# Kernel optimization log

Hardware: AMD Instinct MI355X
Metric: run time of the kernel (lower is better)

The kernel has to match this reference:

```python
import jax, jax.numpy as jnp
import numpy as np
from jax.scipy.special import ndtr

TABLE_RANGE = 128
LRELU_SLOPE = 0.2


def ste_round(x):
    # round(x) - detach(x) + x : straight-through estimator (eval path uses floor(x+0.5))
    return x + jax.lax.stop_gradient(jnp.floor(x + 0.5) - x)


def block_sample(x, masked):
    """Faithful, efficient version of BlockSample's sparse one-hot 7x7 conv.
    out[b, k*16+i*4+j, y, x] = in[b, k, y+i-3, x+j-2]  (zeros outside; masked kills (i=3,j>=2)).
    Equivalent to gathering 4x4 patches from the input padded by 3, at offset (i, j+1).
    Returns (b*h*w, c, 4, 4)."""
    b, c, h, w = x.shape
    xp = jnp.pad(x, ((0, 0), (0, 0), (3, 3), (3, 3)))
    # 16 static shifted slices -> (b, c, 4, 4, h, w)
    patches = jnp.stack(
        [xp[:, :, i:i + h, j + 1:j + 1 + w] for i in range(4) for j in range(4)], axis=2
    ).reshape(b, c, 4, 4, h, w)
    if masked:
        m = np.ones((4, 4), dtype=np.float32)
        m[3, 2] = 0.0
        m[3, 3] = 0.0
        patches = patches * jnp.asarray(m)[None, None, :, :, None, None]
    # (b, h, w, c, 4, 4) -> (b*h*w, c, 4, 4)
    return patches.transpose(0, 4, 5, 1, 2, 3).reshape(b * h * w, c, 4, 4)


def conv2d(x, w, b, stride):
    y = jax.lax.conv_general_dilated(
        x, w, (stride, stride), ((1, 1), (1, 1)),
        dimension_numbers=('NCHW', 'OIHW', 'NCHW'))
    return y + b[None, :, None, None]


def lrelu(x):
    return jnp.where(x >= 0, x, LRELU_SLOPE * x)


def setup_inputs() -> dict:
    key = jax.random.key(0)
    ks = jax.random.split(key, 8)
    b, c, ch, h, w, dim = 8, 192, 192, 32, 48, 192
    y = jax.random.normal(ks[0], (b, c, h, w), jnp.float32) * 4.0
    h_tilde = jax.random.normal(ks[1], (b, ch, h, w), jnp.float32)
    s = 0.02
    w0 = jax.random.normal(ks[2], (dim, c + ch, 3, 3), jnp.float32) * s
    b0 = jnp.zeros((dim,), jnp.float32)
    w1 = jax.random.normal(ks[3], (dim, dim, 3, 3), jnp.float32) * s
    b1 = jnp.zeros((dim,), jnp.float32)
    w2 = jax.random.normal(ks[4], (dim, dim, 3, 3), jnp.float32) * s
    b2 = jnp.zeros((dim,), jnp.float32)
    fc_w = jax.random.normal(ks[5], (2 * c, dim * 2 * 2), jnp.float32) * s
    fc_b = jnp.zeros((2 * c,), jnp.float32)
    return {'y': y, 'h_tilde': h_tilde, 'w0': w0, 'b0': b0, 'w1': w1, 'b1': b1,
            'w2': w2, 'b2': b2, 'fc_w': fc_w, 'fc_b': fc_b}


def reference(y, h_tilde, w0, b0, w1, b1, w2, b2, fc_w, fc_b):
    b, c, h, w = y.shape
    # quantize latents (NoiseQuant eval path with STE gradient)
    y_q = jnp.clip(ste_round(y), -TABLE_RANGE, TABLE_RANGE - 1)
    ys = block_sample(y_q, masked=True)        # (b*h*w, c, 4, 4)
    hs = block_sample(h_tilde, masked=False)   # (b*h*w, ch, 4, 4)
    merged = jnp.concatenate([ys, hs], axis=1)
    # PredictionModel_Context.transform
    t = lrelu(conv2d(merged, w0, b0, 1))       # (N, dim, 4, 4)
    t = lrelu(conv2d(t, w1, b1, 2))            # (N, dim, 2, 2)
    t = lrelu(conv2d(t, w2, b2, 1))            # (N, dim, 2, 2)
    ctx = t.reshape(t.shape[0], -1) @ fc_w.T + fc_b  # (N, 2c)
    hyper_mu = ctx[:, :c].reshape(b, h, w, c).transpose(0, 3, 1, 2)
    hyper_sigma = jnp.exp(ctx[:, c:]).reshape(b, h, w, c).transpose(0, 3, 1, 2)
    # GaussianModel: CDF(upper) - CDF(lower), clamped
    upper = (y_q - hyper_mu + 0.5) / hyper_sigma
    lower = (y_q - hyper_mu - 0.5) / hyper_sigma
    likelihood = jnp.clip(ndtr(upper) - ndtr(lower), 1e-12, None)
    return likelihood
```

## Files before the change

### kernel.cpp

```cpp
#include <hip/hip_runtime.h>
#include <math.h>

constexpr int Bb   = 8;
constexpr int Cc   = 192;
constexpr int Hh   = 32;
constexpr int Ww   = 48;
constexpr int NPIX = 1536;
constexpr int S    = 12288;

typedef __attribute__((ext_vector_type(8))) short s16x8;
typedef __attribute__((ext_vector_type(4))) float f32x4;
typedef unsigned short u16;

#define LRELU(v) ((v) >= 0.0f ? (v) : 0.2f * (v))

__device__ __forceinline__ u16 f2b(float x) {
    __bf16 h = (__bf16)x;
    return *reinterpret_cast<u16*>(&h);
}

__global__ __launch_bounds__(256) void k_quantT(
    const float* __restrict__ y, const float* __restrict__ ht,
    u16* __restrict__ XT)
{
    __shared__ float ld[32][33];
    const int tx = threadIdx.x, ty = threadIdx.y;
    const int p0 = blockIdx.x * 32, c0 = blockIdx.y * 32;
    const int img = blockIdx.z >> 1, src = blockIdx.z & 1;
    const float* sp = (src ? ht : y) + (size_t)img * 192 * NPIX;
    #pragma unroll
    for (int k = 0; k < 4; ++k) {
        float v = sp[(size_t)(c0 + ty + 8 * k) * NPIX + p0 + tx];
        if (!src) v = fminf(fmaxf(floorf(v + 0.5f), -128.0f), 127.0f);
        ld[ty + 8 * k][tx] = v;
    }
    __syncthreads();
    #pragma unroll
    for (int k = 0; k < 4; ++k)
        XT[((size_t)img * NPIX + p0 + ty + 8 * k) * 384 + src * 192 + c0 + tx] =
            f2b(ld[tx][ty + 8 * k]);
}

__global__ void k_prep_w0nk(const float* __restrict__ w, u16* __restrict__ wt) {
    int i = blockIdx.x * 256 + threadIdx.x;
    if (i >= 1728 * 384) return;
    int n = i / 384, ic = i % 384;
    int k = n / 192, oc = n % 192;
    wt[i] = f2b(w[(oc * 384 + ic) * 9 + k]);
}
__global__ void k_prep_w1pk(const float* __restrict__ w, u16* __restrict__ wt) {
    const int posflat[25] = {0,1,4,5, 1,2,3,5,6,7, 4,5,8,9,12,13,
                             5,6,7,9,10,11,13,14,15};
    int i = blockIdx.x * 256 + threadIdx.x;
    if (i >= 921600) return;
    int z, r, K, sbase;
    if      (i < 147456) { z = 0; r = i;          K = 768;  sbase = 0;  }
    else if (i < 368640) { z = 1; r = i - 147456; K = 1152; sbase = 4;  }
    else if (i < 589824) { z = 2; r = i - 368640; K = 1152; sbase = 10; }
    else                 { z = 3; r = i - 589824; K = 1728; sbase = 16; }
    int n = r / K, k = r % K;
    int slab = k / 192, ic = k % 192;
    int pos = posflat[sbase + slab];
    int py = pos >> 2, px = pos & 3;
    int ki = py - 2 * (z >> 1) + 1, kj = px - 2 * (z & 1) + 1;
    wt[i] = f2b(w[(n * 192 + ic) * 9 + ki * 3 + kj]);
}
__global__ void k_prep_w2pk(const float* __restrict__ w, u16* __restrict__ wt) {
    int i = blockIdx.x * 256 + threadIdx.x;
    if (i >= 589824) return;
    int z = i / 147456, r = i % 147456;
    int n = r / 768, k = r % 768;
    int pos = k / 192, ic = k % 192;
    int ki = (pos >> 1) - (z >> 1) + 1, kj = (pos & 1) - (z & 1) + 1;
    wt[i] = f2b(w[(n * 192 + ic) * 9 + ki * 3 + kj]);
}
__global__ void k_prep_fcpk(const float* __restrict__ w, u16* __restrict__ wt) {
    int i = blockIdx.x * 256 + threadIdx.x;
    if (i >= 384 * 768) return;
    int o = i / 768, fp = i % 768;
    int q = fp / 192, oc = fp % 192;
    wt[i] = f2b(w[o * 768 + oc * 4 + q]);
}

__global__ __launch_bounds__(256) void k_hgemm(
    const u16* __restrict__ XT, const u16* __restrict__ W,
    float* __restrict__ Hf, float* __restrict__ Hy)
{
    __shared__ u16 As[128 * 40];
    __shared__ u16 Bs[64 * 40];
    const int tid = threadIdx.x;
    const int wave = tid >> 6, lane = tid & 63;
    const int wm = wave >> 1, wn = wave & 1;
    const int l15 = lane & 15, lk = lane >> 4;
    const int n0 = blockIdx.x * 64, s0 = blockIdx.y * 128;

    f32x4 acc[4][2], snap[4][2];
    #pragma unroll
    for (int a = 0; a < 4; ++a)
        #pragma unroll
        for (int b = 0; b < 2; ++b) { acc[a][b] = (f32x4){0,0,0,0}; snap[a][b] = (f32x4){0,0,0,0}; }

    for (int k0 = 0; k0 < 384; k0 += 32) {
        if (k0 == 192) {
            #pragma unroll
            for (int a = 0; a < 4; ++a)
                #pragma unroll
                for (int b = 0; b < 2; ++b) snap[a][b] = acc[a][b];
        }
        #pragma unroll
        for (int i = tid; i < 768; i += 256) {
            if (i < 512) {
                int row = i >> 2, c = i & 3;
                *reinterpret_cast<uint4*>(&As[row * 40 + c * 8]) =
                    *reinterpret_cast<const uint4*>(&XT[(size_t)(s0 + row) * 384 + k0 + c * 8]);
            } else {
                int j = i - 512, row = j >> 2, c = j & 3;
                *reinterpret_cast<uint4*>(&Bs[row * 40 + c * 8]) =
                    *reinterpret_cast<const uint4*>(&W[(size_t)(n0 + row) * 384 + k0 + c * 8]);
            }
        }
        __syncthreads();
        s16x8 af[4], bf[2];
        #pragma unroll
        for (int mi = 0; mi < 4; ++mi)
            af[mi] = *reinterpret_cast<const s16x8*>(&As[(wm * 64 + mi * 16 + l15) * 40 + lk * 8]);
        #pragma unroll
        for (int ni = 0; ni < 2; ++ni)
            bf[ni] = *reinterpret_cast<const s16x8*>(&Bs[(wn * 32 + ni * 16 + l15) * 40 + lk * 8]);
        #pragma unroll
        for (int mi = 0; mi < 4; ++mi)
            #pragma unroll
            for (int ni = 0; ni < 2; ++ni)
                acc[mi][ni] = __builtin_amdgcn_mfma_f32_16x16x32_bf16(af[mi], bf[ni], acc[mi][ni], 0, 0, 0);
        __syncthreads();
    }
    #pragma unroll
    for (int mi = 0; mi < 4; ++mi)
        #pragma unroll
        for (int r = 0; r < 4; ++r) {
            int srow = s0 + wm * 64 + mi * 16 + lk * 4 + r;
            #pragma unroll
            for (int ni = 0; ni < 2; ++ni) {
                int nc = n0 + wn * 32 + ni * 16 + l15;
                Hf[(size_t)srow * 1728 + nc] = acc[mi][ni][r];
                if (n0 >= 576) Hy[(size_t)srow * 1152 + nc - 576] = snap[mi][ni][r];
            }
        }
}

struct TDm { int K[4]; int woff[4]; int yoff[4]; int pm[4][9]; };

__global__ __launch_bounds__(256) void k_mgemm(
    const u16* __restrict__ X, int sx,
    const u16* __restrict__ Wb, const float* __restrict__ bias,
    void* __restrict__ Yb, int sy, int mode, TDm d)
{
    __shared__ u16 As[128 * 40];
    __shared__ u16 Bs[64 * 40];
    const int z = blockIdx.z;
    const int K = d.K[z];
    const u16* W = Wb + d.woff[z];
    const int tid = threadIdx.x;
    const int wave = tid >> 6, lane = tid & 63;
    const int wm = wave >> 1, wn = wave & 1;
    const int l15 = lane & 15, lk = lane >> 4;
    const int n0 = blockIdx.x * 64, s0 = blockIdx.y * 128;

    f32x4 acc[4][2];
    #pragma unroll
    for (int a = 0; a < 4; ++a)
        #pragma unroll
        for (int b = 0; b < 2; ++b) acc[a][b] = (f32x4){0,0,0,0};

    for (int k0 = 0; k0 < K; k0 += 32) {
        const int colA0 = d.pm[z][k0 / 192] * 192 + (k0 % 192);
        #pragma unroll
        for (int i = tid; i < 768; i += 256) {
            if (i < 512) {
                int row = i >> 2, c = i & 3;
                *reinterpret_cast<uint4*>(&As[row * 40 + c * 8]) =
                    *reinterpret_cast<const uint4*>(&X[(size_t)(s0 + row) * sx + colA0 + c * 8]);
            } else {
                int j = i - 512, row = j >> 2, c = j & 3;
                *reinterpret_cast<uint4*>(&Bs[row * 40 + c * 8]) =
                    *reinterpret_cast<const uint4*>(&W[(size_t)(n0 + row) * K + k0 + c * 8]);
            }
        }
        __syncthreads();
        s16x8 af[4], bf[2];
        #pragma unroll
        for (int mi = 0; mi < 4; ++mi)
            af[mi] = *reinterpret_cast<const s16x8*>(&As[(wm * 64 + mi * 16 + l15) * 40 + lk * 8]);
        #pragma unroll
        for (int ni = 0; ni < 2; ++ni)
            bf[ni] = *reinterpret_cast<const s16x8*>(&Bs[(wn * 32 + ni * 16 + l15) * 40 + lk * 8]);
        #pragma unroll
        for (int mi = 0; mi < 4; ++mi)
            #pragma unroll
            for (int ni = 0; ni < 2; ++ni)
                acc[mi][ni] = __builtin_amdgcn_mfma_f32_16x16x32_bf16(af[mi], bf[ni], acc[mi][ni], 0, 0, 0);
        __syncthreads();
    }
    #pragma unroll
    for (int mi = 0; mi < 4; ++mi)
        #pragma unroll
        for (int r = 0; r < 4; ++r) {
            int srow = s0 + wm * 64 + mi * 16 + lk * 4 + r;
            #pragma unroll
            for (int ni = 0; ni < 2; ++ni) {
                int nc = n0 + wn * 32 + ni * 16 + l15;
                float v = acc[mi][ni][r] + bias[nc];
                if (mode == 0) {
                    v = LRELU(v);
                    ((u16*)Yb)[(size_t)srow * sy + d.yoff[z] + nc] = f2b(v);
                } else {
                    ((float*)Yb)[(size_t)srow * sy + d.yoff[z] + nc] = v;
                }
            }
        }
}

__global__ __launch_bounds__(192) void k_asm(
    const float* __restrict__ Hf, const float* __restrict__ Hy,
    const float* __restrict__ b0, u16* __restrict__ t0)
{
    const int cpx = gridDim.x >> 3;
    const int bid = (blockIdx.x & 7) * cpx + (blockIdx.x >> 3);
    const int oc = threadIdx.x;
    const float bias = b0[oc];
    for (int si = 0; si < 8; ++si) {
        const int s = bid * 8 + si;
        const int imgbase = (s / NPIX) * NPIX;
        const int p = s % NPIX;
        const int yy = p / Ww, xx = p % Ww;
        float acc[16];
        #pragma unroll
        for (int i = 0; i < 16; ++i) acc[i] = bias;
        #pragma unroll
        for (int py = 0; py < 4; ++py) {
            #pragma unroll
            for (int px = 0; px < 4; ++px) {
                int Y = yy + py - 3, X = xx + px - 2;
                if ((unsigned)Y < (unsigned)Hh && (unsigned)X < (unsigned)Ww) {
                    const float* hp = Hf + (size_t)(imgbase + Y * Ww + X) * 1728 + oc;
                    #pragma unroll
                    for (int dy = -1; dy <= 1; ++dy) {
                        int oy = py - dy; if (oy < 0 || oy > 3) continue;
                        #pragma unroll
                        for (int dx = -1; dx <= 1; ++dx) {
                            int ox = px - dx; if (ox < 0 || ox > 3) continue;
                            acc[oy * 4 + ox] += hp[((dy + 1) * 3 + dx + 1) * 192];
                        }
                    }
                }
            }
        }
        {
            const float* yp = Hy + (size_t)s * 1152 + oc;
            #pragma unroll
            for (int dy = 0; dy <= 1; ++dy)
                #pragma unroll
                for (int dx = -1; dx <= 1; ++dx)
                    acc[(3 - dy) * 4 + (2 - dx)] -= yp[(dy * 3 + dx + 1) * 192];
        }
        if (xx + 1 < Ww) {
            const float* yp = Hy + (size_t)(s + 1) * 1152 + oc;
            #pragma unroll
            for (int dy = 0; dy <= 1; ++dy)
                #pragma unroll
                for (int dx = 0; dx <= 1; ++dx)
                    acc[(3 - dy) * 4 + (3 - dx)] -= yp[(dy * 3 + dx + 1) * 192];
        }
        u16* tr = t0 + (size_t)s * 3072 + oc;
        #pragma unroll
        for (int pos = 0; pos < 16; ++pos) tr[pos * 192] = f2b(LRELU(acc[pos]));
    }
}

__global__ void k_like(const float* __restrict__ ctx, const u16* __restrict__ XT,
                       float* __restrict__ like)
{
    int i = blockIdx.x * 256 + threadIdx.x;
    if (i >= 192 * S) return;
    int s = i / 192, c = i % 192;
    u16 qb = XT[(size_t)s * 384 + c];
    unsigned qu = (unsigned)qb << 16;
    float q  = __uint_as_float(qu);
    float mu = ctx[(size_t)s * 384 + c];
    float sg = expf(ctx[(size_t)s * 384 + 192 + c]);
    float inv = 1.0f / sg;
    float up = (q - mu + 0.5f) * inv;
    float lo = (q - mu - 0.5f) * inv;
    const float kc = 0.70710678118654752f;
    float lk = 0.5f * erfcf(-up * kc) - 0.5f * erfcf(-lo * kc);
    like[i] = fmaxf(lk, 1e-12f);
}

__global__ __launch_bounds__(256) void k_outT(
    const float* __restrict__ like, float* __restrict__ out)
{
    __shared__ float ld[32][33];
    const int tx = threadIdx.x, ty = threadIdx.y;
    const int p0 = blockIdx.x * 32, c0 = blockIdx.y * 32;
    const int img = blockIdx.z;
    #pragma unroll
    for (int k = 0; k < 4; ++k)
        ld[ty + 8 * k][tx] = like[((size_t)img * NPIX + p0 + ty + 8 * k) * 192 + c0 + tx];
    __syncthreads();
    #pragma unroll
    for (int k = 0; k < 4; ++k)
        out[((size_t)img * 192 + c0 + ty + 8 * k) * NPIX + p0 + tx] = ld[tx][ty + 8 * k];
}

extern "C" void kernel_launch(void* const* d_in, const int* in_sizes, int n_in,
                              void* d_out, int out_size, void* d_ws, size_t ws_size,
                              hipStream_t stream) {
    const float* y    = (const float*)d_in[0];
    const float* ht   = (const float*)d_in[1];
    const float* w0   = (const float*)d_in[2];
    const float* b0   = (const float*)d_in[3];
    const float* w1   = (const float*)d_in[4];
    const float* b1   = (const float*)d_in[5];
    const float* w2   = (const float*)d_in[6];
    const float* b2   = (const float*)d_in[7];
    const float* fcw  = (const float*)d_in[8];
    const float* fcb  = (const float*)d_in[9];
    float* out = (float*)d_out;

    char* ws = (char*)d_ws;
    u16*   XT   = (u16*)(ws);
    u16*   w0nk = (u16*)(ws + 9437184);
    u16*   w1pk = (u16*)(ws + 10764288);
    u16*   w2pk = (u16*)(ws + 12607488);
    u16*   fcpk = (u16*)(ws + 13787136);
    float* Hf   = (float*)(ws + 14376960);
    float* Hy   = (float*)(ws + 99311616);
    u16*   t0   = (u16*)(ws + 155934720);
    u16*   t1   = (u16*)Hy;
    u16*   t2   = (u16*)(ws + 99311616 + 18874368);
    float* ctx  = Hf;
    float* like = (float*)(ws + 14376960 + 18874368);

    k_quantT<<<dim3(48, 6, 16), dim3(32, 8), 0, stream>>>(y, ht, XT);
    k_prep_w0nk<<<(1728 * 384 + 255) / 256, 256, 0, stream>>>(w0, w0nk);
    k_prep_w1pk<<<(921600 + 255) / 256, 256, 0, stream>>>(w1, w1pk);
    k_prep_w2pk<<<(589824 + 255) / 256, 256, 0, stream>>>(w2, w2pk);
    k_prep_fcpk<<<(384 * 768 + 255) / 256, 256, 0, stream>>>(fcw, fcpk);

    TDm dB = {}, dC = {}, dD = {};
    const int KB[4]   = {768, 1152, 1152, 1728};
    const int wB[4]   = {0, 147456, 368640, 589824};
    const int pmB[4][9] = {
        {0,1,4,5,0,0,0,0,0},
        {1,2,3,5,6,7,0,0,0},
        {4,5,8,9,12,13,0,0,0},
        {5,6,7,9,10,11,13,14,15}};
    for (int q = 0; q < 4; ++q) {
        dB.K[q] = KB[q]; dB.woff[q] = wB[q]; dB.yoff[q] = q * 192;
        for (int j = 0; j < 9; ++j) dB.pm[q][j] = pmB[q][j];
        dC.K[q] = 768; dC.woff[q] = q * 147456; dC.yoff[q] = q * 192;
        for (int j = 0; j < 4; ++j) dC.pm[q][j] = j;
        dD.K[q] = 768; dD.woff[q] = 0; dD.yoff[q] = 0;
        for (int j = 0; j < 4; ++j) dD.pm[q][j] = j;
    }

    k_hgemm<<<dim3(27, 96), 256, 0, stream>>>(XT, w0nk, Hf, Hy);
    k_asm<<<1536, 192, 0, stream>>>(Hf, Hy, b0, t0);
    k_mgemm<<<dim3(3, 96, 4), 256, 0, stream>>>(t0, 3072, w1pk, b1, t1, 768, 0, dB);
    k_mgemm<<<dim3(3, 96, 4), 256, 0, stream>>>(t1, 768, w2pk, b2, t2, 768, 0, dC);
    k_mgemm<<<dim3(6, 96, 1), 256, 0, stream>>>(t2, 768, fcpk, fcb, ctx, 384, 1, dD);
    k_like<<<(192 * S + 255) / 256, 256, 0, stream>>>(ctx, XT, like);
    k_outT<<<dim3(48, 6, 8), dim3(32, 8), 0, stream>>>(like, out);
}
```

Baseline: 413.9 us.

## Widen GEMM tiles with direct-to-LDS loads and store conv0 partials in bf16

The shared GEMM kernel now uses 128x192 tiles with K steps of 64 and an XOR-swizzled LDS layout. Tiles are filled with global_load_lds direct-to-LDS copies instead of register staging. The separate conv0 GEMM is replaced by two launches of the generic GEMM, one for the full-K partials and one for the y-only partials with its own weight pack. Both write bf16 instead of fp32, and the assembly kernel reads packed bf16 pairs, which halves that intermediate traffic. The second conv is merged into one wide-N launch with a replicated bias. This cuts memory traffic and raises reuse per tile, at the cost of more register pressure, larger LDS use and bf16 rounding of the partial sums.

```diff
diff --git a/kernel.cpp b/kernel.cpp
--- a/kernel.cpp
+++ b/kernel.cpp
@@ -11,12 +11,19 @@
 typedef __attribute__((ext_vector_type(8))) short s16x8;
 typedef __attribute__((ext_vector_type(4))) float f32x4;
 typedef unsigned short u16;
+typedef unsigned int   u32;
 
 #define LRELU(v) ((v) >= 0.0f ? (v) : 0.2f * (v))
 
 __device__ __forceinline__ u16 f2b(float x) {
     __bf16 h = (__bf16)x;
     return *reinterpret_cast<u16*>(&h);
+}
+
+__device__ __forceinline__ void gload(const u16* g, u16* l) {
+    __builtin_amdgcn_global_load_lds(
+        (const __attribute__((address_space(1))) unsigned int*)g,
+        (__attribute__((address_space(3))) unsigned int*)l, 16, 0, 0);
 }
 
 __global__ __launch_bounds__(256) void k_quantT(
@@ -46,6 +53,13 @@
     if (i >= 1728 * 384) return;
     int n = i / 384, ic = i % 384;
     int k = n / 192, oc = n % 192;
+    wt[i] = f2b(w[(oc * 384 + ic) * 9 + k]);
+}
+__global__ void k_prep_w0yk(const float* __restrict__ w, u16* __restrict__ wt) {
+    int i = blockIdx.x * 256 + threadIdx.x;
+    if (i >= 1152 * 192) return;
+    int n = i / 192, ic = i % 192;
+    int oc = n % 192, k = n / 192 + 3;
     wt[i] = f2b(w[(oc * 384 + ic) * 9 + k]);
 }
 __global__ void k_prep_w1pk(const float* __restrict__ w, u16* __restrict__ wt) {
@@ -81,71 +95,9 @@
     int q = fp / 192, oc = fp % 192;
     wt[i] = f2b(w[o * 768 + oc * 4 + q]);
 }
-
-__global__ __launch_bounds__(256) void k_hgemm(
-    const u16* __restrict__ XT, const u16* __restrict__ W,
-    float* __restrict__ Hf, float* __restrict__ Hy)
-{
-    __shared__ u16 As[128 * 40];
-    __shared__ u16 Bs[64 * 40];
-    const int tid = threadIdx.x;
-    const int wave = tid >> 6, lane = tid & 63;
-    const int wm = wave >> 1, wn = wave & 1;
-    const int l15 = lane & 15, lk = lane >> 4;
-    const int n0 = blockIdx.x * 64, s0 = blockIdx.y * 128;
-
-    f32x4 acc[4][2], snap[4][2];
-    #pragma unroll
-    for (int a = 0; a < 4; ++a)
-        #pragma unroll
-        for (int b = 0; b < 2; ++b) { acc[a][b] = (f32x4){0,0,0,0}; snap[a][b] = (f32x4){0,0,0,0}; }
-
-    for (int k0 = 0; k0 < 384; k0 += 32) {
-        if (k0 == 192) {
-            #pragma unroll
-            for (int a = 0; a < 4; ++a)
-                #pragma unroll
-                for (int b = 0; b < 2; ++b) snap[a][b] = acc[a][b];
-        }
-        #pragma unroll
-        for (int i = tid; i < 768; i += 256) {
-            if (i < 512) {
-                int row = i >> 2, c = i & 3;
-                *reinterpret_cast<uint4*>(&As[row * 40 + c * 8]) =
-                    *reinterpret_cast<const uint4*>(&XT[(size_t)(s0 + row) * 384 + k0 + c * 8]);
-            } else {
-                int j = i - 512, row = j >> 2, c = j & 3;
-                *reinterpret_cast<uint4*>(&Bs[row * 40 + c * 8]) =
-                    *reinterpret_cast<const uint4*>(&W[(size_t)(n0 + row) * 384 + k0 + c * 8]);
-            }
-        }
-        __syncthreads();
-        s16x8 af[4], bf[2];
-        #pragma unroll
-        for (int mi = 0; mi < 4; ++mi)
-            af[mi] = *reinterpret_cast<const s16x8*>(&As[(wm * 64 + mi * 16 + l15) * 40 + lk * 8]);
-        #pragma unroll
-        for (int ni = 0; ni < 2; ++ni)
-            bf[ni] = *reinterpret_cast<const s16x8*>(&Bs[(wn * 32 + ni * 16 + l15) * 40 + lk * 8]);
-        #pragma unroll
-        for (int mi = 0; mi < 4; ++mi)
-            #pragma unroll
-            for (int ni = 0; ni < 2; ++ni)
-                acc[mi][ni] = __builtin_amdgcn_mfma_f32_16x16x32_bf16(af[mi], bf[ni], acc[mi][ni], 0, 0, 0);
-        __syncthreads();
-    }
-    #pragma unroll
-    for (int mi = 0; mi < 4; ++mi)
-        #pragma unroll
-        for (int r = 0; r < 4; ++r) {
-            int srow = s0 + wm * 64 + mi * 16 + lk * 4 + r;
-            #pragma unroll
-            for (int ni = 0; ni < 2; ++ni) {
-                int nc = n0 + wn * 32 + ni * 16 + l15;
-                Hf[(size_t)srow * 1728 + nc] = acc[mi][ni][r];
-                if (n0 >= 576) Hy[(size_t)srow * 1152 + nc - 576] = snap[mi][ni][r];
-            }
-        }
+__global__ void k_prep_b2rep(const float* __restrict__ b, float* __restrict__ o) {
+    int i = blockIdx.x * 256 + threadIdx.x;
+    if (i < 768) o[i] = b[i % 192];
 }
 
 struct TDm { int K[4]; int woff[4]; int yoff[4]; int pm[4][9]; };
@@ -155,125 +107,155 @@
     const u16* __restrict__ Wb, const float* __restrict__ bias,
     void* __restrict__ Yb, int sy, int mode, TDm d)
 {
-    __shared__ u16 As[128 * 40];
-    __shared__ u16 Bs[64 * 40];
+    __shared__ u16 As[128 * 64];
+    __shared__ u16 Bs[192 * 64];
     const int z = blockIdx.z;
     const int K = d.K[z];
     const u16* W = Wb + d.woff[z];
     const int tid = threadIdx.x;
-    const int wave = tid >> 6, lane = tid & 63;
-    const int wm = wave >> 1, wn = wave & 1;
+    const int wv = tid >> 6, lane = tid & 63;
+    const int wm = wv & 1, wn = wv >> 1;
     const int l15 = lane & 15, lk = lane >> 4;
-    const int n0 = blockIdx.x * 64, s0 = blockIdx.y * 128;
-
-    f32x4 acc[4][2];
+    const int lr = lane >> 3, lc = lane & 7;
+    const int sc = lc ^ lr;
+    const int n0 = blockIdx.x * 192, s0 = blockIdx.y * 128;
+
+    f32x4 acc[4][6];
     #pragma unroll
     for (int a = 0; a < 4; ++a)
         #pragma unroll
-        for (int b = 0; b < 2; ++b) acc[a][b] = (f32x4){0,0,0,0};
-
-    for (int k0 = 0; k0 < K; k0 += 32) {
-        const int colA0 = d.pm[z][k0 / 192] * 192 + (k0 % 192);
-        #pragma unroll
-        for (int i = tid; i < 768; i += 256) {
-            if (i < 512) {
-                int row = i >> 2, c = i & 3;
-                *reinterpret_cast<uint4*>(&As[row * 40 + c * 8]) =
-                    *reinterpret_cast<const uint4*>(&X[(size_t)(s0 + row) * sx + colA0 + c * 8]);
+        for (int b = 0; b < 6; ++b) acc[a][b] = (f32x4){0, 0, 0, 0};
+
+    int slab = 0, kin = 0;
+    for (int k0 = 0; k0 < K; k0 += 64) {
+        const int colA0 = d.pm[z][slab] * 192 + kin;
+        for (int st = wv; st < 40; st += 4) {
+            if (st < 16) {
+                const u16* g = X + (size_t)(s0 + st * 8 + lr) * sx + colA0 + sc * 8;
+                gload(g, &As[st * 512]);
             } else {
-                int j = i - 512, row = j >> 2, c = j & 3;
-                *reinterpret_cast<uint4*>(&Bs[row * 40 + c * 8]) =
-                    *reinterpret_cast<const uint4*>(&W[(size_t)(n0 + row) * K + k0 + c * 8]);
+                const int bs = st - 16;
+                const u16* g = W + (size_t)(n0 + bs * 8 + lr) * K + k0 + sc * 8;
+                gload(g, &Bs[bs * 512]);
             }
         }
         __syncthreads();
-        s16x8 af[4], bf[2];
-        #pragma unroll
-        for (int mi = 0; mi < 4; ++mi)
-            af[mi] = *reinterpret_cast<const s16x8*>(&As[(wm * 64 + mi * 16 + l15) * 40 + lk * 8]);
-        #pragma unroll
-        for (int ni = 0; ni < 2; ++ni)
-            bf[ni] = *reinterpret_cast<const s16x8*>(&Bs[(wn * 32 + ni * 16 + l15) * 40 + lk * 8]);
-        #pragma unroll
-        for (int mi = 0; mi < 4; ++mi)
-            #pragma unroll
-            for (int ni = 0; ni < 2; ++ni)
-                acc[mi][ni] = __builtin_amdgcn_mfma_f32_16x16x32_bf16(af[mi], bf[ni], acc[mi][ni], 0, 0, 0);
+
+        #pragma unroll
+        for (int ks = 0; ks < 2; ++ks) {
+            s16x8 af[4], bf[6];
+            #pragma unroll
+            for (int mi = 0; mi < 4; ++mi) {
+                const int r = wm * 64 + mi * 16 + l15;
+                af[mi] = *reinterpret_cast<const s16x8*>(
+                    &As[r * 64 + (((ks * 4 + lk) * 8) ^ ((l15 & 7) << 3))]);
+            }
+            #pragma unroll
+            for (int ni = 0; ni < 6; ++ni) {
+                const int r = wn * 96 + ni * 16 + l15;
+                bf[ni] = *reinterpret_cast<const s16x8*>(
+                    &Bs[r * 64 + (((ks * 4 + lk) * 8) ^ ((l15 & 7) << 3))]);
+            }
+            #pragma unroll
+            for (int mi = 0; mi < 4; ++mi)
+                #pragma unroll
+                for (int ni = 0; ni < 6; ++ni)
+                    acc[mi][ni] = __builtin_amdgcn_mfma_f32_16x16x32_bf16(
+                        af[mi], bf[ni], acc[mi][ni], 0, 0, 0);
+        }
         __syncthreads();
+        kin += 64; if (kin == 192) { kin = 0; ++slab; }
     }
+
     #pragma unroll
     for (int mi = 0; mi < 4; ++mi)
         #pragma unroll
         for (int r = 0; r < 4; ++r) {
-            int srow = s0 + wm * 64 + mi * 16 + lk * 4 + r;
-            #pragma unroll
-            for (int ni = 0; ni < 2; ++ni) {
-                int nc = n0 + wn * 32 + ni * 16 + l15;
-                float v = acc[mi][ni][r] + bias[nc];
+            const int srow = s0 + wm * 64 + mi * 16 + lk * 4 + r;
+            #pragma unroll
+            for (int ni = 0; ni < 6; ++ni) {
+                const int ng = n0 + wn * 96 + ni * 16 + l15;
+                float v = acc[mi][ni][r];
+                if (mode != 2) v += bias[ng];
                 if (mode == 0) {
                     v = LRELU(v);
-                    ((u16*)Yb)[(size_t)srow * sy + d.yoff[z] + nc] = f2b(v);
+                    ((u16*)Yb)[(size_t)srow * sy + d.yoff[z] + ng] = f2b(v);
+                } else if (mode == 1) {
+                    ((float*)Yb)[(size_t)srow * sy + ng] = v;
                 } else {
-                    ((float*)Yb)[(size_t)srow * sy + d.yoff[z] + nc] = v;
+                    ((u16*)Yb)[(size_t)srow * sy + ng] = f2b(v);
                 }
             }
         }
 }
 
 __global__ __launch_bounds__(192) void k_asm(
-    const float* __restrict__ Hf, const float* __restrict__ Hy,
+    const u16* __restrict__ Hf, const u16* __restrict__ Hy,
     const float* __restrict__ b0, u16* __restrict__ t0)
 {
     const int cpx = gridDim.x >> 3;
     const int bid = (blockIdx.x & 7) * cpx + (blockIdx.x >> 3);
-    const int oc = threadIdx.x;
-    const float bias = b0[oc];
-    for (int si = 0; si < 8; ++si) {
-        const int s = bid * 8 + si;
+    const int t = threadIdx.x % 96, h = threadIdx.x / 96;
+    const float bias0 = b0[2 * t], bias1 = b0[2 * t + 1];
+    const u32* HF = (const u32*)Hf;
+    const u32* HY = (const u32*)Hy;
+    u32* T0 = (u32*)t0;
+    for (int si = 0; si < 4; ++si) {
+        const int s = bid * 8 + h * 4 + si;
         const int imgbase = (s / NPIX) * NPIX;
         const int p = s % NPIX;
         const int yy = p / Ww, xx = p % Ww;
-        float acc[16];
-        #pragma unroll
-        for (int i = 0; i < 16; ++i) acc[i] = bias;
-        #pragma unroll
-        for (int py = 0; py < 4; ++py) {
+        float a0[16], a1[16];
+        #pragma unroll
+        for (int i = 0; i < 16; ++i) { a0[i] = bias0; a1[i] = bias1; }
+        #pragma unroll
+        for (int py = 0; py < 4; ++py)
             #pragma unroll
             for (int px = 0; px < 4; ++px) {
                 int Y = yy + py - 3, X = xx + px - 2;
                 if ((unsigned)Y < (unsigned)Hh && (unsigned)X < (unsigned)Ww) {
-                    const float* hp = Hf + (size_t)(imgbase + Y * Ww + X) * 1728 + oc;
+                    const u32* hp = HF + (size_t)(imgbase + Y * Ww + X) * 864 + t;
                     #pragma unroll
                     for (int dy = -1; dy <= 1; ++dy) {
                         int oy = py - dy; if (oy < 0 || oy > 3) continue;
                         #pragma unroll
                         for (int dx = -1; dx <= 1; ++dx) {
                             int ox = px - dx; if (ox < 0 || ox > 3) continue;
-                            acc[oy * 4 + ox] += hp[((dy + 1) * 3 + dx + 1) * 192];
+                            u32 v = hp[((dy + 1) * 3 + dx + 1) * 96];
+                            a0[oy * 4 + ox] += __uint_as_float(v << 16);
+                            a1[oy * 4 + ox] += __uint_as_float(v & 0xffff0000u);
                         }
                     }
                 }
             }
-        }
         {
-            const float* yp = Hy + (size_t)s * 1152 + oc;
+            const u32* yp = HY + (size_t)s * 576 + t;
             #pragma unroll
             for (int dy = 0; dy <= 1; ++dy)
                 #pragma unroll
-                for (int dx = -1; dx <= 1; ++dx)
-                    acc[(3 - dy) * 4 + (2 - dx)] -= yp[(dy * 3 + dx + 1) * 192];
+                for (int dx = -1; dx <= 1; ++dx) {
+                    u32 v = yp[(dy * 3 + dx + 1) * 96];
+                    a0[(3 - dy) * 4 + (2 - dx)] -= __uint_as_float(v << 16);
+                    a1[(3 - dy) * 4 + (2 - dx)] -= __uint_as_float(v & 0xffff0000u);
+                }
         }
         if (xx + 1 < Ww) {
-            const float* yp = Hy + (size_t)(s + 1) * 1152 + oc;
+            const u32* yp = HY + (size_t)(s + 1) * 576 + t;
             #pragma unroll
             for (int dy = 0; dy <= 1; ++dy)
                 #pragma unroll
-                for (int dx = 0; dx <= 1; ++dx)
-                    acc[(3 - dy) * 4 + (3 - dx)] -= yp[(dy * 3 + dx + 1) * 192];
-        }
-        u16* tr = t0 + (size_t)s * 3072 + oc;
-        #pragma unroll
-        for (int pos = 0; pos < 16; ++pos) tr[pos * 192] = f2b(LRELU(acc[pos]));
+                for (int dx = 0; dx <= 1; ++dx) {
+                    u32 v = yp[(dy * 3 + dx + 1) * 96];
+                    a0[(3 - dy) * 4 + (3 - dx)] -= __uint_as_float(v << 16);
+                    a1[(3 - dy) * 4 + (3 - dx)] -= __uint_as_float(v & 0xffff0000u);
+                }
+        }
+        u32* tr = T0 + (size_t)s * 1536 + t;
+        #pragma unroll
+        for (int pos = 0; pos < 16; ++pos) {
+            float v0 = LRELU(a0[pos]), v1 = LRELU(a1[pos]);
+            tr[pos * 96] = (u32)f2b(v0) | ((u32)f2b(v1) << 16);
+        }
     }
 }
 
@@ -283,9 +265,7 @@
     int i = blockIdx.x * 256 + threadIdx.x;
     if (i >= 192 * S) return;
     int s = i / 192, c = i % 192;
-    u16 qb = XT[(size_t)s * 384 + c];
-    unsigned qu = (unsigned)qb << 16;
-    float q  = __uint_as_float(qu);
+    float q  = __uint_as_float((u32)XT[(size_t)s * 384 + c] << 16);
     float mu = ctx[(size_t)s * 384 + c];
     float sg = expf(ctx[(size_t)s * 384 + 192 + c]);
     float inv = 1.0f / sg;
@@ -328,28 +308,34 @@
     float* out = (float*)d_out;
 
     char* ws = (char*)d_ws;
-    u16*   XT   = (u16*)(ws);
-    u16*   w0nk = (u16*)(ws + 9437184);
-    u16*   w1pk = (u16*)(ws + 10764288);
-    u16*   w2pk = (u16*)(ws + 12607488);
-    u16*   fcpk = (u16*)(ws + 13787136);
-    float* Hf   = (float*)(ws + 14376960);
-    float* Hy   = (float*)(ws + 99311616);
-    u16*   t0   = (u16*)(ws + 155934720);
-    u16*   t1   = (u16*)Hy;
-    u16*   t2   = (u16*)(ws + 99311616 + 18874368);
-    float* ctx  = Hf;
-    float* like = (float*)(ws + 14376960 + 18874368);
+    u16*   XT    = (u16*)(ws);
+    u16*   w0nk  = (u16*)(ws + 9437184);
+    u16*   w0yk  = (u16*)(ws + 10764288);
+    u16*   w1pk  = (u16*)(ws + 11206656);
+    u16*   w2pk  = (u16*)(ws + 13049856);
+    u16*   fcpk  = (u16*)(ws + 14229504);
+    float* b2rep = (float*)(ws + 14819328);
+    u16*   Hf    = (u16*)(ws + 14822400);
+    u16*   Hy    = (u16*)(ws + 57289728);
+    u16*   t0    = (u16*)(ws + 85601280);
+    u16*   t1    = (u16*)(ws + 161098752);
+    u16*   t2    = (u16*)(ws + 179973120);
+    float* ctx   = (float*)(ws + 198847488);
+    float* like  = (float*)(ws + 217721856);
 
     k_quantT<<<dim3(48, 6, 16), dim3(32, 8), 0, stream>>>(y, ht, XT);
     k_prep_w0nk<<<(1728 * 384 + 255) / 256, 256, 0, stream>>>(w0, w0nk);
+    k_prep_w0yk<<<(1152 * 192 + 255) / 256, 256, 0, stream>>>(w0, w0yk);
     k_prep_w1pk<<<(921600 + 255) / 256, 256, 0, stream>>>(w1, w1pk);
     k_prep_w2pk<<<(589824 + 255) / 256, 256, 0, stream>>>(w2, w2pk);
     k_prep_fcpk<<<(384 * 768 + 255) / 256, 256, 0, stream>>>(fcw, fcpk);
-
-    TDm dB = {}, dC = {}, dD = {};
-    const int KB[4]   = {768, 1152, 1152, 1728};
-    const int wB[4]   = {0, 147456, 368640, 589824};
+    k_prep_b2rep<<<3, 256, 0, stream>>>(b2, b2rep);
+
+    TDm dH = {}, dHy = {}, dB = {}, dC = {}, dD = {};
+    dH.K[0] = 384;  dH.pm[0][0] = 0; dH.pm[0][1] = 1;
+    dHy.K[0] = 192; dHy.pm[0][0] = 0;
+    const int KB[4] = {768, 1152, 1152, 1728};
+    const int wB[4] = {0, 147456, 368640, 589824};
     const int pmB[4][9] = {
         {0,1,4,5,0,0,0,0,0},
         {1,2,3,5,6,7,0,0,0},
@@ -358,17 +344,16 @@
     for (int q = 0; q < 4; ++q) {
         dB.K[q] = KB[q]; dB.woff[q] = wB[q]; dB.yoff[q] = q * 192;
         for (int j = 0; j < 9; ++j) dB.pm[q][j] = pmB[q][j];
-        dC.K[q] = 768; dC.woff[q] = q * 147456; dC.yoff[q] = q * 192;
-        for (int j = 0; j < 4; ++j) dC.pm[q][j] = j;
-        dD.K[q] = 768; dD.woff[q] = 0; dD.yoff[q] = 0;
-        for (int j = 0; j < 4; ++j) dD.pm[q][j] = j;
     }
-
-    k_hgemm<<<dim3(27, 96), 256, 0, stream>>>(XT, w0nk, Hf, Hy);
+    dC.K[0] = 768; for (int j = 0; j < 4; ++j) dC.pm[0][j] = j;
+    dD.K[0] = 768; for (int j = 0; j < 4; ++j) dD.pm[0][j] = j;
+
+    k_mgemm<<<dim3(9, 96, 1), 256, 0, stream>>>(XT, 384, w0nk, b0,   Hf, 1728, 2, dH);
+    k_mgemm<<<dim3(6, 96, 1), 256, 0, stream>>>(XT, 384, w0yk, b0,   Hy, 1152, 2, dHy);
     k_asm<<<1536, 192, 0, stream>>>(Hf, Hy, b0, t0);
-    k_mgemm<<<dim3(3, 96, 4), 256, 0, stream>>>(t0, 3072, w1pk, b1, t1, 768, 0, dB);
-    k_mgemm<<<dim3(3, 96, 4), 256, 0, stream>>>(t1, 768, w2pk, b2, t2, 768, 0, dC);
-    k_mgemm<<<dim3(6, 96, 1), 256, 0, stream>>>(t2, 768, fcpk, fcb, ctx, 384, 1, dD);
+    k_mgemm<<<dim3(1, 96, 4), 256, 0, stream>>>(t0, 3072, w1pk, b1,    t1, 768, 0, dB);
+    k_mgemm<<<dim3(4, 96, 1), 256, 0, stream>>>(t1, 768,  w2pk, b2rep, t2, 768, 0, dC);
+    k_mgemm<<<dim3(2, 96, 1), 256, 0, stream>>>(t2, 768,  fcpk, fcb,  ctx, 384, 1, dD);
     k_like<<<(192 * S + 255) / 256, 256, 0, stream>>>(ctx, XT, like);
     k_outT<<<dim3(48, 6, 8), dim3(32, 8), 0, stream>>>(like, out);
 }
```

Result: slower. 436.3 us (+5.4%).
